# Performance work log

Hardware: AMD Instinct MI355X
Metric: run time of the kernel (lower is better)

The kernel has to match this reference:

```python
import jax, jax.numpy as jnp
import numpy as np

B, L, D = 32, 512, 128          # batch, seq_len, d_model (= num graph nodes N)
E, HS, DTR, U = 64, 64, 4, 32   # d_proj_E, d_proj_H (state), dt_rank, d_proj_U
R, K, DE, NH = 3, 3, 10, 4      # mamba layers, cheb order, d_e, heads
EPS = 1e-5


def _ln(x, g, b):
    m = jnp.mean(x, -1, keepdims=True)
    v = jnp.mean((x - m) ** 2, -1, keepdims=True)
    return (x - m) / jnp.sqrt(v + EPS) * g + b


def _mamba(x, in_w, conv_w, conv_b, xproj_w, dt_w, dt_b, Alog, Dp, out_w):
    b, l, _ = x.shape
    xz = x @ in_w                                  # (b,l,2E)
    xp, res = xz[..., :E], xz[..., E:]
    xc = jnp.transpose(xp, (0, 2, 1))              # (b,E,l)
    # causal depthwise conv: torch pads both sides by d_conv-1 then slices [:l]
    xc = jax.lax.conv_general_dilated(
        xc, conv_w, (1,), [(conv_w.shape[-1] - 1, 0)],
        dimension_numbers=('NCH', 'OIH', 'NCH'), feature_group_count=E)
    xc = xc + conv_b[None, :, None]
    xp = jax.nn.silu(jnp.transpose(xc, (0, 2, 1)))  # (b,l,E)
    xdbl = xp @ xproj_w                             # (b,l,DTR+2*HS)
    delta = jax.nn.softplus(xdbl[..., :DTR] @ dt_w + dt_b)        # (b,l,E)
    Bm = xdbl[..., DTR:DTR + HS]                                   # (b,l,HS)
    Cm = xdbl[..., DTR + HS:]                                      # (b,l,HS)
    A = -jnp.exp(Alog)                                             # (E,HS)
    dA = jnp.exp(delta[..., None] * A)                             # (b,l,E,HS)
    dBu = delta[..., None] * Bm[:, :, None, :] * xp[..., None]     # (b,l,E,HS)

    def step(s, t):
        dA_t, dBu_t, C_t = t
        s = dA_t * s + dBu_t
        return s, jnp.einsum('bdn,bn->bd', s, C_t)

    _, ys = jax.lax.scan(step, jnp.zeros((b, E, HS), x.dtype),
                         (jnp.swapaxes(dA, 0, 1), jnp.swapaxes(dBu, 0, 1),
                          jnp.swapaxes(Cm, 0, 1)))
    y = jnp.swapaxes(ys, 0, 1) + xp * Dp
    y = y * jax.nn.sigmoid(res)
    return y @ out_w


def _forward(x, mb_in_w, mb_conv_w, mb_conv_b, mb_xproj_w, mb_dt_w, mb_dt_b,
             mb_Alog, mb_D, mb_out_w, ln1_g, ln1_b, ln2_g, ln2_b,
             ffn_w1, ffn_b1, ffn_w2, ffn_b2,
             psi_emb, psi, W_q, W_k, attn_alpha, F_w, f_b, head_mix,
             head_w, head_b):
    # ---- bidirectional Mamba stack ----
    for i in range(R):
        f, bk = 2 * i, 2 * i + 1
        Y1 = _mamba(x, mb_in_w[f], mb_conv_w[f], mb_conv_b[f], mb_xproj_w[f],
                    mb_dt_w[f], mb_dt_b[f], mb_Alog[f], mb_D[f], mb_out_w[f])
        Y2 = jnp.flip(_mamba(jnp.flip(x, 1), mb_in_w[bk], mb_conv_w[bk],
                             mb_conv_b[bk], mb_xproj_w[bk], mb_dt_w[bk],
                             mb_dt_b[bk], mb_Alog[bk], mb_D[bk], mb_out_w[bk]), 1)
        Y3 = _ln(x + Y1 + Y2, ln1_g[i], ln1_b[i])
        Yp = jax.nn.relu(Y3 @ ffn_w1[i] + ffn_b1[i]) @ ffn_w2[i] + ffn_b2[i]
        x = _ln(Yp + Y3, ln2_g[i], ln2_b[i])
    h = jnp.transpose(x, (0, 2, 1))                # (B, N=D, L)
    # ---- MAGAC (deterministic single MC sample, eval, no edge drop) ----
    diff = psi_emb[:, None, :] - psi_emb[None, :, :]
    A_g = jax.nn.softmax(jnp.exp(-psi * jnp.sum(diff * diff, -1)), axis=1)
    Q = jnp.einsum('nd,dhm->nhm', psi_emb, W_q)
    Kt = jnp.einsum('nd,dhm->nhm', psi_emb, W_k)
    attn = jax.nn.softmax(jnp.einsum('nhd,mhd->hnm', Q, Kt)
                          / jnp.sqrt(jnp.asarray(DE, x.dtype)), axis=-1)
    alpha = jax.nn.sigmoid(attn_alpha)
    A_effs = alpha * A_g[None] + (1.0 - alpha) * attn   # (H,N,N)
    mix = jax.nn.softmax(head_mix)
    I = jnp.eye(D, dtype=x.dtype)
    out = jnp.zeros((x.shape[0], D), x.dtype)
    for hh in range(NH):
        A = A_effs[hh]
        sup = [I, A]
        for _ in range(2, K + 1):
            sup.append(2.0 * A @ sup[-1] - sup[-2])
        S = jnp.stack(sup, 0)                             # (K+1,N,N)
        Wf = jnp.einsum('nd,dkl->nkl', psi_emb, F_w[hh])  # (N,K+1,L)
        bf = psi_emb @ f_b[hh]                            # (N,)
        out_h = jnp.einsum('knm,bml,nkl->bn', S, h, Wf) + bf
        out = out + mix[hh] * out_h
    log_var = jnp.zeros_like(out)
    pred = out @ head_w + head_b                          # (B,1)
    return pred, log_var


def setup_inputs() -> dict:
    key = jax.random.key(0)
    ks = iter(jax.random.split(key, 40))
    nrm = lambda shp, s=0.05: (jax.random.normal(next(ks), shp, jnp.float32) * s)
    M = 2 * R
    base_Alog = jnp.log(jnp.arange(1, HS + 1, dtype=jnp.float32))
    inp = {
        'x': jax.random.normal(next(ks), (B, L, D), jnp.float32),
        'mb_in_w': nrm((M, D, 2 * E)),
        'mb_conv_w': nrm((M, E, 1, 3), 0.2),
        'mb_conv_b': jnp.zeros((M, E), jnp.float32),
        'mb_xproj_w': nrm((M, E, DTR + 2 * HS)),
        'mb_dt_w': nrm((M, DTR, E), 0.2),
        'mb_dt_b': jnp.zeros((M, E), jnp.float32),
        'mb_Alog': jnp.tile(base_Alog[None, None, :], (M, E, 1)),
        'mb_D': jnp.ones((M, E), jnp.float32),
        'mb_out_w': nrm((M, E, D)),
        'ln1_g': jnp.ones((R, D), jnp.float32),
        'ln1_b': jnp.zeros((R, D), jnp.float32),
        'ln2_g': jnp.ones((R, D), jnp.float32),
        'ln2_b': jnp.zeros((R, D), jnp.float32),
        'ffn_w1': nrm((R, D, U)),
        'ffn_b1': jnp.zeros((R, U), jnp.float32),
        'ffn_w2': nrm((R, U, D)),
        'ffn_b2': jnp.zeros((R, D), jnp.float32),
        'psi_emb': jax.random.normal(next(ks), (D, DE), jnp.float32),
        'psi': jnp.asarray(1.0, jnp.float32),
        'W_q': jax.random.normal(next(ks), (DE, NH, DE), jnp.float32),
        'W_k': jax.random.normal(next(ks), (DE, NH, DE), jnp.float32),
        'attn_alpha': jnp.asarray(0.5, jnp.float32),
        'F_w': nrm((NH, DE, K + 1, L), 0.05),
        'f_b': nrm((NH, DE), 1.0),
        'head_mix': jnp.ones((NH,), jnp.float32),
        'head_w': nrm((D, 1)),
        'head_b': jnp.zeros((1,), jnp.float32),
    }
    return inp


def reference(x, mb_in_w, mb_conv_w, mb_conv_b, mb_xproj_w, mb_dt_w, mb_dt_b,
              mb_Alog, mb_D, mb_out_w, ln1_g, ln1_b, ln2_g, ln2_b,
              ffn_w1, ffn_b1, ffn_w2, ffn_b2,
              psi_emb, psi, W_q, W_k, attn_alpha, F_w, f_b, head_mix,
              head_w, head_b):
    return _forward(x, mb_in_w, mb_conv_w, mb_conv_b, mb_xproj_w, mb_dt_w,
                    mb_dt_b, mb_Alog, mb_D, mb_out_w, ln1_g, ln1_b, ln2_g,
                    ln2_b, ffn_w1, ffn_b1, ffn_w2, ffn_b2, psi_emb, psi,
                    W_q, W_k, attn_alpha, F_w, f_b, head_mix, head_w, head_b)
```

## Files before the change

kernel.cpp:

```cpp
#include <hip/hip_runtime.h>
#include <hip/hip_bf16.h>


#define B_ 32
#define L_ 512
#define D_ 128
#define E_ 64
#define HS_ 64

#define OFF_X     0u
#define OFF_XZF   2097152u
#define OFF_XZB   4194304u
#define OFF_XPF   6291456u
#define OFF_XPB   7340032u
#define OFF_PKF   8388608u
#define OFF_PKB   10485760u
#define OFF_XBCF  12582912u
#define OFF_WFT   13631488u
#define OFF_XBCB  14680064u
#define OFF_STT   15728640u
#define OFF_AEFF  15990784u
#define OFF_YSF   16777216u
#define OFF_YSB   17825792u
#define OFF_V     2097152u
#define OFF_PART  12582912u
#define OFF_RED1  16777216u

__device__ __forceinline__ float sigf(float x) { return 1.f / (1.f + __expf(-x)); }
__device__ __forceinline__ unsigned int bf16r(float x) {
    unsigned int u = __float_as_uint(x);
    return (u + 0x7fffu + ((u >> 16) & 1u)) >> 16;
}

__device__ void role_wf(int bx0, int tid, const float* __restrict__ psi,
                        const float* __restrict__ F_w, float* __restrict__ WfT)
{
    const int idx = bx0 * 256 + tid;
    const int n = idx & 127, l = (idx >> 7) & 511, k = (idx >> 16) & 3, h = idx >> 18;
    float acc = 0.f;
#pragma unroll
    for (int d = 0; d < 10; ++d)
        acc = fmaf(psi[n * 10 + d], F_w[((h * 10 + d) * 4 + k) * 512 + l], acc);
    WfT[idx] = acc;
}

__device__ void role_qkaeff(int bx0, int tid, const float* __restrict__ psi,
                            const float* __restrict__ psis, const float* __restrict__ W_q,
                            const float* __restrict__ W_k, const float* __restrict__ attn_a,
                            float* __restrict__ Aeff, float* __restrict__ StT,
                            float* sQ2 , float* red2 )
{
    const int half = tid >> 7, mcol = tid & 127;
    const int unit = bx0 * 2 + half;
    const int h = unit >> 7, n = unit & 127;
    float Kreg[10];
#pragma unroll
    for (int d = 0; d < 10; ++d) Kreg[d] = 0.f;
#pragma unroll
    for (int d0 = 0; d0 < 10; ++d0) {
        const float pv = psi[mcol * 10 + d0];
#pragma unroll
        for (int d = 0; d < 10; ++d) Kreg[d] = fmaf(pv, W_k[(d0 * 4 + h) * 10 + d], Kreg[d]);
    }
    if (mcol < 10) {
        float qd = 0.f;
        for (int d0 = 0; d0 < 10; ++d0)
            qd = fmaf(psi[n * 10 + d0], W_q[(d0 * 4 + h) * 10 + mcol], qd);
        sQ2[half * 16 + mcol] = qd;
    }
    __syncthreads();
    float d2 = 0.f;
#pragma unroll
    for (int d = 0; d < 10; ++d) { const float df = psi[n * 10 + d] - psi[mcol * 10 + d]; d2 = fmaf(df, df, d2); }
    const float gv = __expf(-psis[0] * d2);
    float qv = 0.f;
#pragma unroll
    for (int d = 0; d < 10; ++d) qv = fmaf(sQ2[half * 16 + d], Kreg[d], qv);
    qv *= 0.3162277660168379332f;
    float* rd = red2 + half * 128;
    float r;
    rd[mcol] = gv; __syncthreads();
    for (int s = 64; s >= 1; s >>= 1) { if (mcol < s) rd[mcol] = fmaxf(rd[mcol], rd[mcol + s]); __syncthreads(); }
    r = rd[0]; __syncthreads();
    const float eg = __expf(gv - r);
    rd[mcol] = eg; __syncthreads();
    for (int s = 64; s >= 1; s >>= 1) { if (mcol < s) rd[mcol] += rd[mcol + s]; __syncthreads(); }
    const float gsum = rd[0]; __syncthreads();
    rd[mcol] = qv; __syncthreads();
    for (int s = 64; s >= 1; s >>= 1) { if (mcol < s) rd[mcol] = fmaxf(rd[mcol], rd[mcol + s]); __syncthreads(); }
    r = rd[0]; __syncthreads();
    const float eq = __expf(qv - r);
    rd[mcol] = eq; __syncthreads();
    for (int s = 64; s >= 1; s >>= 1) { if (mcol < s) rd[mcol] += rd[mcol + s]; __syncthreads(); }
    const float qsum = rd[0];
    const float al = sigf(attn_a[0]);
    const float aeff = al * (eg / gsum) + (1.f - al) * (eq / qsum);
    Aeff[h * 16384 + n * 128 + mcol] = aeff;
    StT[((h * 4 + 1) * 128 + mcol) * 128 + n] = aeff;
    StT[((h * 4 + 0) * 128 + mcol) * 128 + n] = (mcol == n) ? 1.f : 0.f;
}

__device__ void role_cheb(int bx0, int tid, const float* __restrict__ Aeff,
                          float* __restrict__ StT, int kk)
{
    const int h = bx0 >> 6;
    const int m0 = ((bx0 & 63) << 1) + (tid >> 7);
    const int n = tid & 127;
    const float* Ar = Aeff + h * 16384 + n * 128;
    const float* Sp = StT + ((h * 4 + kk - 1) * 128 + m0) * 128;
    float acc = 0.f;
#pragma unroll 8
    for (int p = 0; p < 128; ++p) acc = fmaf(Ar[p], Sp[p], acc);
    const float s2 = StT[((h * 4 + kk - 2) * 128 + m0) * 128 + n];
    StT[((h * 4 + kk) * 128 + m0) * 128 + n] = 2.f * acc - s2;
}

__global__ __launch_bounds__(256) void gemm_in2_kernel(
    const float* __restrict__ X, const float* __restrict__ WF, const float* __restrict__ WB,
    float* __restrict__ xzF, float* __restrict__ xzB)
{
    __shared__ float sxT[128][36];
    __shared__ float sw[2][16][128];
    const int tid = threadIdx.x;
    const int r0 = blockIdx.x * 32;
    for (int q = tid; q < 1024; q += 256) {
        const int r = q >> 5, k4 = q & 31;
        const float4 v = *(const float4*)&X[(size_t)(r0 + r) * 128 + k4 * 4];
        sxT[k4 * 4 + 0][r] = v.x; sxT[k4 * 4 + 1][r] = v.y;
        sxT[k4 * 4 + 2][r] = v.z; sxT[k4 * 4 + 3][r] = v.w;
    }
    const int wv = tid >> 6, lane = tid & 63;
    const int d = wv >> 1, ch = wv & 1;
    const int r4 = lane >> 4, c16 = lane & 15;
    float4 acc[8];
#pragma unroll
    for (int j = 0; j < 8; ++j) acc[j] = float4{0.f, 0.f, 0.f, 0.f};
    for (int ko = 0; ko < 128; ko += 16) {
        __syncthreads();
        for (int q = tid; q < 1024; q += 256) {
            const int dd = q >> 9, kk = (q >> 5) & 15, c4 = q & 31;
            *(float4*)&sw[dd][kk][c4 * 4] =
                *(const float4*)&((dd ? WB : WF)[(ko + kk) * 128 + c4 * 4]);
        }
        __syncthreads();
#pragma unroll
        for (int kk = 0; kk < 16; ++kk) {
            const float4 w4 = *(const float4*)&sw[d][kk][ch * 64 + c16 * 4];
            const float4 xa = *(const float4*)&sxT[ko + kk][r4 * 8];
            const float4 xb = *(const float4*)&sxT[ko + kk][r4 * 8 + 4];
            const float xs[8] = {xa.x, xa.y, xa.z, xa.w, xb.x, xb.y, xb.z, xb.w};
#pragma unroll
            for (int j = 0; j < 8; ++j) {
                acc[j].x = fmaf(xs[j], w4.x, acc[j].x);
                acc[j].y = fmaf(xs[j], w4.y, acc[j].y);
                acc[j].z = fmaf(xs[j], w4.z, acc[j].z);
                acc[j].w = fmaf(xs[j], w4.w, acc[j].w);
            }
        }
    }
    float* xz = d ? xzB : xzF;
#pragma unroll
    for (int j = 0; j < 8; ++j) {
        *(float4*)&xz[(r0 + r4 * 8 + j) * 128 + ch * 64 + c16 * 4] = acc[j];
    }
}

__global__ __launch_bounds__(256) void prep4_kernel(
    const float* __restrict__ xzF_, const float* __restrict__ xzB_,
    const float* __restrict__ conv_w, const float* __restrict__ conv_b,
    const float* __restrict__ xproj_w, const float* __restrict__ dt_w,
    const float* __restrict__ dt_b, int layer,
    float* __restrict__ xpF_, float* __restrict__ xpB_,
    unsigned int* __restrict__ xbcF_, unsigned int* __restrict__ xbcB_,
    float* __restrict__ pkF_, float* __restrict__ pkB_,
    const float* __restrict__ psi, const float* __restrict__ F_w, float* __restrict__ WfT,
    const float* __restrict__ Aeff, float* __restrict__ StT)
{
    __shared__ float sW[8448];
    __shared__ float sxp4[4][64][4];
    __shared__ float sdl4[4][4][4];
    const int tid = threadIdx.x, wv = tid >> 6, lane = tid & 63;
    if (blockIdx.x >= 2048) {
        const int bx0 = blockIdx.x - 2048;
        if (layer == 0) role_wf(bx0, tid, psi, F_w, WfT);
        else            role_cheb(bx0, tid, Aeff, StT, 3);
        return;
    }
    const int dir = (int)(blockIdx.x >= 1024);
    const int r0 = (blockIdx.x & 1023) * 16;
    const int b = r0 >> 9;
    const int m = layer * 2 + dir;
    const float* Wg = xproj_w + m * 8448;
    for (int q = tid; q < 2112; q += 256) ((float4*)sW)[q] = ((const float4*)Wg)[q];
    const float* xz = dir ? xzB_ : xzF_;
    float* xp  = dir ? xpB_  : xpF_;
    unsigned int* xbc = dir ? xbcB_ : xbcF_;
    float* pkx = dir ? pkB_  : pkF_;
    const float* cw = conv_w + m * 192 + lane * 3;
    const float cw0 = cw[0], cw1 = cw[1], cw2 = cw[2];
    const float cb  = conv_b[m * 64 + lane];
    const float dtb = dt_b[m * 64 + lane];
    const float* dwp = dt_w + m * 256;
    const float dw0 = dwp[lane], dw1 = dwp[64 + lane], dw2 = dwp[128 + lane], dw3 = dwp[192 + lane];
    float uu[4];
#pragma unroll
    for (int it = 0; it < 4; ++it) {
        const int row = r0 + wv * 4 + it;
        const int l = row & 511;
        const int l1 = dir ? l + 1 : l - 1;
        const int l2 = dir ? l + 2 : l - 2;
        float acc = cb;
        const float x0 = xz[(size_t)row * 128 + lane];
        const float x1 = (l1 >= 0 && l1 < 512) ? xz[(size_t)(b * 512 + l1) * 128 + lane] : 0.f;
        const float x2 = (l2 >= 0 && l2 < 512) ? xz[(size_t)(b * 512 + l2) * 128 + lane] : 0.f;
        acc += cw0 * x2 + cw1 * x1 + cw2 * x0;
        const float u = acc * sigf(acc);
        xp[row * 64 + lane] = u;
        uu[it] = u;
    }
    *(float4*)&sxp4[wv][lane][0] = float4{uu[0], uu[1], uu[2], uu[3]};
    __syncthreads();
    const int jdt = lane & 3;
    float aB[4] = {0.f, 0.f, 0.f, 0.f};
    float aC[4] = {0.f, 0.f, 0.f, 0.f};
    float adt[4] = {0.f, 0.f, 0.f, 0.f};
#pragma unroll 4
    for (int k = 0; k < 64; ++k) {
        const float wB = sW[k * 132 + 4 + lane];
        const float wC = sW[k * 132 + 68 + lane];
        const float wd = sW[k * 132 + jdt];
        const float4 xv = *(const float4*)&sxp4[wv][k][0];
        aB[0] = fmaf(xv.x, wB, aB[0]); aC[0] = fmaf(xv.x, wC, aC[0]); adt[0] = fmaf(xv.x, wd, adt[0]);
        aB[1] = fmaf(xv.y, wB, aB[1]); aC[1] = fmaf(xv.y, wC, aC[1]); adt[1] = fmaf(xv.y, wd, adt[1]);
        aB[2] = fmaf(xv.z, wB, aB[2]); aC[2] = fmaf(xv.z, wC, aC[2]); adt[2] = fmaf(xv.z, wd, adt[2]);
        aB[3] = fmaf(xv.w, wB, aB[3]); aC[3] = fmaf(xv.w, wC, aC[3]); adt[3] = fmaf(xv.w, wd, adt[3]);
    }
#pragma unroll
    for (int it = 0; it < 4; ++it) {
        const int row = r0 + wv * 4 + it;
        xbc[row * 64 + lane] = (bf16r(aC[it]) << 16) | bf16r(aB[it]);
        if (lane < 4) sdl4[wv][it][lane] = adt[it];
    }
#pragma unroll
    for (int it = 0; it < 4; ++it) {
        const int row = r0 + wv * 4 + it;
        float dpre = fmaf(sdl4[wv][it][0], dw0, dtb);
        dpre = fmaf(sdl4[wv][it][1], dw1, dpre);
        dpre = fmaf(sdl4[wv][it][2], dw2, dpre);
        dpre = fmaf(sdl4[wv][it][3], dw3, dpre);
        const float dlt = (dpre > 20.f) ? dpre : log1pf(__expf(dpre));
        ((float2*)pkx)[row * 64 + lane] = float2{dlt, dlt * uu[it]};
    }
}

__global__ __launch_bounds__(256, 4) void scan8_kernel(
    const unsigned int* __restrict__ xbcF, const unsigned int* __restrict__ xbcB,
    const float* __restrict__ pkF, const float* __restrict__ pkB,
    const float* __restrict__ AlogF, const float* __restrict__ AlogB,
    float* __restrict__ ysF, float* __restrict__ ysB,
    const float* __restrict__ psi, const float* __restrict__ psis,
    const float* __restrict__ W_q, const float* __restrict__ W_k,
    const float* __restrict__ attn_a, float* __restrict__ Aeff, float* __restrict__ StT)
{
    __shared__ unsigned int sbc[2][1024];
    __shared__ float spk[2][4][16][2];
    __shared__ float ytile[4][16][68];
    const int tid = threadIdx.x, wv = tid >> 6, lane = tid & 63;
    const int bx = blockIdx.x;
    if (bx >= 1024) {
        role_qkaeff(bx - 1024, tid, psi, psis, W_q, W_k, attn_a, Aeff, StT,
                    (float*)&sbc[1][0], (float*)&sbc[0][0]);
        return;
    }
    const int db = bx & 63;
    const int dir = db >> 5;
    const int b   = db & 31;
    const int e0  = (bx >> 6) * 4;
    const int e   = e0 + wv;
    const unsigned int* xbc = dir ? xbcB : xbcF;
    const float* pk  = dir ? pkB  : pkF;
    const float* Aw  = dir ? AlogB : AlogF;
    float* ys = dir ? ysB : ysF;
    const float a2 = -__expf(Aw[e * 64 + lane]) * 1.4426950408889634f;
    float s = 0.f;
    float* yrow = ys + (size_t)(b * 64 + e) * 512;

    const int psl = tid & 15, pw_ = tid >> 4;

#define STG_LOAD(RS)                                                              \
    {                                                                             \
        nb = *(const uint4*)(xbc + (size_t)(RS) * 64 + tid * 4);                  \
        if (tid < 64)                                                             \
            npp = *(const float2*)(pk + (size_t)((RS) + psl) * 128 + (e0 + pw_) * 2); \
    }
#define STG_WRITE(BUF)                                                            \
    {                                                                             \
        *(uint4*)(&sbc[BUF][tid * 4]) = nb;                                       \
        if (tid < 64) *(float2*)(&spk[BUF][pw_][psl][0]) = npp;                   \
    }

#define SCAN16(REV)                                                               \
    {                                                                             \
        const unsigned int* bc = &sbc[cur][0];                                    \
        const float* pq = &spk[cur][wv][0][0];                                    \
        _Pragma("unroll")                                                         \
        for (int j = 0; j < 8; ++j) {                                             \
            const int pj = (REV) ? 7 - j : j;                                     \
            const float4 pk4 = *(const float4*)(pq + pj * 4);                     \
            const int sA = (REV) ? 15 - 2 * j : 2 * j;                            \
            const int sB = (REV) ? 14 - 2 * j : 2 * j + 1;                        \
            const float dlA = (REV) ? pk4.z : pk4.x;                              \
            const float duA = (REV) ? pk4.w : pk4.y;                              \
            const float dlB = (REV) ? pk4.x : pk4.z;                              \
            const float duB = (REV) ? pk4.y : pk4.w;                              \
            const unsigned int bA = bc[sA * 64 + lane];                           \
            const float BnA = __uint_as_float(bA << 16);                          \
            const float CnA = __uint_as_float(bA & 0xffff0000u);                  \
            s = fmaf(__builtin_amdgcn_exp2f(dlA * a2), s, duA * BnA);             \
            ytile[wv][sA][lane] = s * CnA;                                        \
            const unsigned int bB = bc[sB * 64 + lane];                           \
            const float BnB = __uint_as_float(bB << 16);                          \
            const float CnB = __uint_as_float(bB & 0xffff0000u);                  \
            s = fmaf(__builtin_amdgcn_exp2f(dlB * a2), s, duB * BnB);             \
            ytile[wv][sB][lane] = s * CnB;                                        \
        }                                                                         \
    }

    {
        uint4 nb; float2 npp;
        const int rs0 = b * 512 + (dir ? 496 : 0);
        STG_LOAD(rs0);
        STG_WRITE(0);
    }
    __syncthreads();

    int cur = 0;
    const int rr = lane & 15, sg = lane >> 4;
    for (int t = 0; t < 32; ++t) {
        uint4 nb; float2 npp;
        const bool more = (t + 1) < 32;
        if (more) {
            const int rs = b * 512 + (dir ? (496 - (t + 1) * 16) : ((t + 1) * 16));
            STG_LOAD(rs);
        }
        if (dir == 0) { SCAN16(0) } else { SCAN16(1) }
        {
            const float* yt = &ytile[wv][rr][sg * 16];
            const float4 A0 = *(const float4*)yt;
            const float4 A1 = *(const float4*)(yt + 4);
            const float4 A2 = *(const float4*)(yt + 8);
            const float4 A3 = *(const float4*)(yt + 12);
            float p = ((A0.x + A0.y) + (A0.z + A0.w)) + ((A1.x + A1.y) + (A1.z + A1.w))
                    + ((A2.x + A2.y) + (A2.z + A2.w)) + ((A3.x + A3.y) + (A3.z + A3.w));
            p += __shfl_xor(p, 16);
            p += __shfl_xor(p, 32);
            if (lane < 16) {
                const int lg = dir ? (496 + rr - t * 16) : (t * 16 + rr);
                yrow[lg] = p;
            }
        }
        if (more) STG_WRITE(cur ^ 1);
        __syncthreads();
        cur ^= 1;
    }
#undef STG_LOAD
#undef STG_WRITE
#undef SCAN16
}

__global__ __launch_bounds__(256, 4) void opfn3_kernel(
    const float* __restrict__ ysF, const float* __restrict__ ysB,
    const float* __restrict__ xpF, const float* __restrict__ xpB,
    const float* __restrict__ xzF, const float* __restrict__ xzB,
    const float* __restrict__ Dp, int layer,
    const float* __restrict__ Xc, const float* __restrict__ out_w,
    const float* __restrict__ W1, const float* __restrict__ b1,
    const float* __restrict__ W2, const float* __restrict__ b2,
    const float* __restrict__ g1, const float* __restrict__ bb1,
    const float* __restrict__ g2, const float* __restrict__ bb2,
    float* __restrict__ xout,
    const float* __restrict__ WFn, const float* __restrict__ WBn,
    float* __restrict__ xzFo, float* __restrict__ xzBo,
    const float* __restrict__ Aeff, float* __restrict__ StT)
{
    __shared__ float smem[9216];
    float* syy = smem;
    float* sw  = smem + 4096;
    float* sh  = smem + 8192;
    const int tid = threadIdx.x;
    if (blockIdx.x >= 512) {
        role_cheb(blockIdx.x - 512, tid, Aeff, StT, 2);
        return;
    }
    const int r0 = blockIdx.x * 32;
    const int b = r0 >> 9, l0 = r0 & 511;
    const int wv = tid >> 6, lane = tid & 63;
    const float* WFp = out_w + (layer * 2) * 8192;
    const float* WBp = out_w + (layer * 2 + 1) * 8192;

    for (int q = tid; q < 1024; q += 256) {
        const int d = q >> 9, ee = (q >> 3) & 63, rq = q & 7;
        const float* ysp = d ? ysB : ysF;
        const float4 v = *(const float4*)&ysp[(size_t)(b * 64 + ee) * 512 + l0 + rq * 4];
        const float dv = Dp[(layer * 2 + d) * 64 + ee];
        const float* xpp = d ? xpB : xpF;
        const float* xzp = d ? xzB : xzF;
        const float vv[4] = {v.x, v.y, v.z, v.w};
#pragma unroll
        for (int j = 0; j < 4; ++j) {
            const int r = rq * 4 + j;
            const int row = r0 + r;
            const float u   = xpp[(size_t)row * 64 + ee];
            const float res = xzp[(size_t)row * 128 + 64 + ee];
            syy[r * 128 + d * 64 + ee] = (vv[j] + u * dv) * sigf(res);
        }
    }
    __syncthreads();

    float acc[8][2];
#pragma unroll
    for (int r = 0; r < 8; ++r) { acc[r][0] = 0.f; acc[r][1] = 0.f; }
#define OPSTEP8(COMP, J)                                                          \
        {                                                                         \
            const float w0 = sw[(kk + (J)) * 128 + lane];                         \
            const float w1 = sw[(kk + (J)) * 128 + lane + 64];                    \
            acc[0][0] = fmaf(y40.COMP, w0, acc[0][0]); acc[0][1] = fmaf(y40.COMP, w1, acc[0][1]); \
            acc[1][0] = fmaf(y41.COMP, w0, acc[1][0]); acc[1][1] = fmaf(y41.COMP, w1, acc[1][1]); \
            acc[2][0] = fmaf(y42.COMP, w0, acc[2][0]); acc[2][1] = fmaf(y42.COMP, w1, acc[2][1]); \
            acc[3][0] = fmaf(y43.COMP, w0, acc[3][0]); acc[3][1] = fmaf(y43.COMP, w1, acc[3][1]); \
            acc[4][0] = fmaf(y44.COMP, w0, acc[4][0]); acc[4][1] = fmaf(y44.COMP, w1, acc[4][1]); \
            acc[5][0] = fmaf(y45.COMP, w0, acc[5][0]); acc[5][1] = fmaf(y45.COMP, w1, acc[5][1]); \
            acc[6][0] = fmaf(y46.COMP, w0, acc[6][0]); acc[6][1] = fmaf(y46.COMP, w1, acc[6][1]); \
            acc[7][0] = fmaf(y47.COMP, w0, acc[7][0]); acc[7][1] = fmaf(y47.COMP, w1, acc[7][1]); \
        }
#define GEMM_CHUNK8(SRC, KO)                                                      \
    _Pragma("unroll")                                                             \
    for (int kk = 0; kk < 32; kk += 4) {                                          \
        const float4 y40 = *(const float4*)&(SRC)[(wv * 8 + 0) * 128 + (KO) + kk];\
        const float4 y41 = *(const float4*)&(SRC)[(wv * 8 + 1) * 128 + (KO) + kk];\
        const float4 y42 = *(const float4*)&(SRC)[(wv * 8 + 2) * 128 + (KO) + kk];\
        const float4 y43 = *(const float4*)&(SRC)[(wv * 8 + 3) * 128 + (KO) + kk];\
        const float4 y44 = *(const float4*)&(SRC)[(wv * 8 + 4) * 128 + (KO) + kk];\
        const float4 y45 = *(const float4*)&(SRC)[(wv * 8 + 5) * 128 + (KO) + kk];\
        const float4 y46 = *(const float4*)&(SRC)[(wv * 8 + 6) * 128 + (KO) + kk];\
        const float4 y47 = *(const float4*)&(SRC)[(wv * 8 + 7) * 128 + (KO) + kk];\
        OPSTEP8(x, 0) OPSTEP8(y, 1) OPSTEP8(z, 2) OPSTEP8(w, 3)                  \
    }
    for (int koi = 0; koi < 4; ++koi) {
        if (koi) __syncthreads();
        for (int q = tid; q < 1024; q += 256) {
            const int kk = q >> 5, c4 = q & 31;
            const int kg = koi * 32 + kk;
            *(float4*)&sw[kk * 128 + c4 * 4] = (kg < 64)
                ? *(const float4*)&WFp[kg * 128 + c4 * 4]
                : *(const float4*)&WBp[(kg - 64) * 128 + c4 * 4];
        }
        __syncthreads();
        GEMM_CHUNK8(syy, koi * 32);
    }
    __syncthreads();
    for (int q = tid; q < 1024; q += 256) ((float4*)sw)[q] = ((const float4*)W1)[q];
#pragma unroll
    for (int r = 0; r < 8; ++r) {
        const int rl = wv * 8 + r;
        const int row = r0 + rl;
        float v0 = acc[r][0] + Xc[(size_t)row * 128 + lane];
        float v1 = acc[r][1] + Xc[(size_t)row * 128 + lane + 64];
        float sum = v0 + v1, sq = v0 * v0 + v1 * v1;
#pragma unroll
        for (int o = 32; o >= 1; o >>= 1) { sum += __shfl_xor(sum, o); sq += __shfl_xor(sq, o); }
        const float mean = sum * (1.f / 128.f);
        const float var = sq * (1.f / 128.f) - mean * mean;
        const float rs = rsqrtf(var + 1e-5f);
        syy[rl * 128 + lane]      = (v0 - mean) * rs * g1[lane] + bb1[lane];
        syy[rl * 128 + lane + 64] = (v1 - mean) * rs * g1[lane + 64] + bb1[lane + 64];
    }
    __syncthreads();
    {
        const int r = tid >> 3, ug = (tid & 7) * 4;
        float h0 = b1[ug], h1 = b1[ug + 1], h2 = b1[ug + 2], h3 = b1[ug + 3];
#pragma unroll 8
        for (int k = 0; k < 128; ++k) {
            const float xv = syy[r * 128 + k];
            h0 = fmaf(xv, sw[k * 32 + ug], h0);
            h1 = fmaf(xv, sw[k * 32 + ug + 1], h1);
            h2 = fmaf(xv, sw[k * 32 + ug + 2], h2);
            h3 = fmaf(xv, sw[k * 32 + ug + 3], h3);
        }
        sh[r * 32 + ug]     = fmaxf(h0, 0.f);
        sh[r * 32 + ug + 1] = fmaxf(h1, 0.f);
        sh[r * 32 + ug + 2] = fmaxf(h2, 0.f);
        sh[r * 32 + ug + 3] = fmaxf(h3, 0.f);
    }
    __syncthreads();
    for (int q = tid; q < 1024; q += 256) ((float4*)sw)[q] = ((const float4*)W2)[q];
    __syncthreads();
    float xr[8][2];
#pragma unroll
    for (int r = 0; r < 8; ++r) {
        const int rl = wv * 8 + r;
        float a0 = b2[lane], a1 = b2[lane + 64];
#pragma unroll 8
        for (int k = 0; k < 32; ++k) {
            const float hv = sh[rl * 32 + k];
            a0 = fmaf(hv, sw[k * 128 + lane], a0);
            a1 = fmaf(hv, sw[k * 128 + lane + 64], a1);
        }
        const float v0 = a0 + syy[rl * 128 + lane];
        const float v1 = a1 + syy[rl * 128 + lane + 64];
        float sum = v0 + v1, sq = v0 * v0 + v1 * v1;
#pragma unroll
        for (int o = 32; o >= 1; o >>= 1) { sum += __shfl_xor(sum, o); sq += __shfl_xor(sq, o); }
        const float mean = sum * (1.f / 128.f);
        const float var = sq * (1.f / 128.f) - mean * mean;
        const float rs = rsqrtf(var + 1e-5f);
        const int row = r0 + rl;
        const float o0 = (v0 - mean) * rs * g2[lane] + bb2[lane];
        const float o1 = (v1 - mean) * rs * g2[lane + 64] + bb2[lane + 64];
        xout[(size_t)row * 128 + lane]      = o0;
        xout[(size_t)row * 128 + lane + 64] = o1;
        xr[r][0] = o0; xr[r][1] = o1;
    }
    if (WFn == nullptr) return;
    __syncthreads();
    float* sxr = syy;
#pragma unroll
    for (int r = 0; r < 8; ++r) {
        sxr[(wv * 8 + r) * 128 + lane]      = xr[r][0];
        sxr[(wv * 8 + r) * 128 + lane + 64] = xr[r][1];
    }
    for (int c = 0; c < 8; ++c) {
        const int dd = c >> 2, ko = (c & 3) * 32;
        const float* Wn = dd ? WBn : WFn;
        for (int q = tid; q < 1024; q += 256) {
            const int kk = q >> 5, c4 = q & 31;
            *(float4*)&sw[kk * 128 + c4 * 4] = *(const float4*)&Wn[(ko + kk) * 128 + c4 * 4];
        }
        __syncthreads();
        if ((c & 3) == 0) {
#pragma unroll
            for (int r = 0; r < 8; ++r) { acc[r][0] = 0.f; acc[r][1] = 0.f; }
        }
        GEMM_CHUNK8(sxr, ko);
        if ((c & 3) == 3) {
            float* xzo = dd ? xzBo : xzFo;
#pragma unroll
            for (int r = 0; r < 8; ++r) {
                const int row = r0 + wv * 8 + r;
                xzo[(size_t)row * 128 + lane]      = acc[r][0];
                xzo[(size_t)row * 128 + lane + 64] = acc[r][1];
            }
        }
        __syncthreads();
    }
#undef OPSTEP8
#undef GEMM_CHUNK8
}

__global__ __launch_bounds__(256) void head_v4_kernel(
    const float* __restrict__ StT, const float* __restrict__ WfT, const float* __restrict__ hmix,
    float* __restrict__ V)
{
    const float m0 = hmix[0], m1 = hmix[1], m2 = hmix[2], m3 = hmix[3];
    const float mxx = fmaxf(fmaxf(m0, m1), fmaxf(m2, m3));
    const float e0 = __expf(m0 - mxx), e1 = __expf(m1 - mxx), e2 = __expf(m2 - mxx), e3 = __expf(m3 - mxx);
    const float inv = 1.f / (e0 + e1 + e2 + e3);
    const float mixv[4] = {e0 * inv, e1 * inv, e2 * inv, e3 * inv};
    const int tid = threadIdx.x;
    const int lt = blockIdx.x & 63, mm = blockIdx.x >> 6;
    const int n4 = tid & 31, mh = tid >> 5;
    const int m = mm * 8 + mh;
    const int l0 = lt * 8, n0 = n4 * 4;
    float4 sv[16];
#pragma unroll
    for (int h = 0; h < 4; ++h) {
        const float mx = mixv[h];
#pragma unroll
        for (int k = 0; k < 4; ++k) {
            const float4 v = *(const float4*)&StT[(size_t)((h * 4 + k) * 128 + m) * 128 + n0];
            sv[h * 4 + k] = float4{v.x * mx, v.y * mx, v.z * mx, v.w * mx};
        }
    }
#pragma unroll
    for (int j = 0; j < 8; ++j) {
        const int l = l0 + j;
        float4 acc = {0.f, 0.f, 0.f, 0.f};
#pragma unroll
        for (int hk = 0; hk < 16; ++hk) {
            const float4 w = *(const float4*)&WfT[(size_t)(hk * 512 + l) * 128 + n0];
            acc.x = fmaf(sv[hk].x, w.x, acc.x);
            acc.y = fmaf(sv[hk].y, w.y, acc.y);
            acc.z = fmaf(sv[hk].z, w.z, acc.z);
            acc.w = fmaf(sv[hk].w, w.w, acc.w);
        }
        *(float4*)&V[(size_t)(l * 128 + m) * 128 + n0] = acc;
    }
}

__global__ __launch_bounds__(256) void head_ctr_kernel(
    const float* __restrict__ Xf, const float* __restrict__ V, float* __restrict__ partial)
{
    __shared__ float sx[32][128];
    const int l = blockIdx.x, tid = threadIdx.x;
    const int n = tid & 127, mh = tid >> 7;
    for (int q = tid; q < 1024; q += 256) {
        const int b = q >> 5, m4 = q & 31;
        *(float4*)&sx[b][m4 * 4] = *(const float4*)&Xf[(size_t)(b * 512 + l) * 128 + m4 * 4];
    }
    __syncthreads();
    float acc[32];
#pragma unroll
    for (int b = 0; b < 32; ++b) acc[b] = 0.f;
    const float* vp = V + (size_t)(l * 128 + mh * 64) * 128 + n;
    for (int mm = 0; mm < 64; ++mm) {
        const float v = vp[(size_t)mm * 128];
        const int m = mh * 64 + mm;
#pragma unroll
        for (int b = 0; b < 32; ++b) acc[b] = fmaf(sx[b][m], v, acc[b]);
    }
#pragma unroll
    for (int b = 0; b < 32; ++b)
        partial[(size_t)((l * 2 + mh) * 32 + b) * 128 + n] = acc[b];
}

__global__ __launch_bounds__(128) void head_red_kernel(
    const float* __restrict__ partial, float* __restrict__ red1)
{
    const int b = blockIdx.x >> 5, cs = blockIdx.x & 31, n = threadIdx.x;
    const float* p = partial + ((size_t)(cs * 32) * 32 + b) * 128 + n;
    float s = 0.f;
#pragma unroll 8
    for (int c = 0; c < 32; ++c) s += p[(size_t)c * 4096];
    red1[(b * 32 + cs) * 128 + n] = s;
}

__global__ __launch_bounds__(128) void head_out_kernel(
    const float* __restrict__ red1, const float* __restrict__ psi,
    const float* __restrict__ f_b, const float* __restrict__ hmix,
    const float* __restrict__ head_w, const float* __restrict__ head_b, float* __restrict__ out)
{
    __shared__ float red[128];
    const int b = blockIdx.x, n = threadIdx.x;
    const float m0 = hmix[0], m1 = hmix[1], m2 = hmix[2], m3 = hmix[3];
    const float mxx = fmaxf(fmaxf(m0, m1), fmaxf(m2, m3));
    const float e0 = __expf(m0 - mxx), e1 = __expf(m1 - mxx), e2 = __expf(m2 - mxx), e3 = __expf(m3 - mxx);
    const float inv = 1.f / (e0 + e1 + e2 + e3);
    const float mixv[4] = {e0 * inv, e1 * inv, e2 * inv, e3 * inv};
    float s = 0.f;
#pragma unroll
    for (int h = 0; h < 4; ++h) {
        float t = 0.f;
#pragma unroll
        for (int d = 0; d < 10; ++d) t = fmaf(psi[n * 10 + d], f_b[h * 10 + d], t);
        s = fmaf(mixv[h], t, s);
    }
#pragma unroll 8
    for (int cs = 0; cs < 32; ++cs) s += red1[(b * 32 + cs) * 128 + n];
    red[n] = s * head_w[n];
    __syncthreads();
    for (int st = 64; st >= 1; st >>= 1) { if (n < st) red[n] += red[n + st]; __syncthreads(); }
    if (n == 0) out[b] = red[0] + head_b[0];
    out[32 + b * 128 + n] = 0.f;
}

extern "C" void kernel_launch(void* const* d_in, const int* in_sizes, int n_in,
                              void* d_out, int out_size, void* d_ws, size_t ws_size,
                              hipStream_t stream) {
    const float* x_in    = (const float*)d_in[0];
    const float* in_w    = (const float*)d_in[1];
    const float* conv_w  = (const float*)d_in[2];
    const float* conv_b  = (const float*)d_in[3];
    const float* xproj_w = (const float*)d_in[4];
    const float* dt_w    = (const float*)d_in[5];
    const float* dt_b    = (const float*)d_in[6];
    const float* Alog    = (const float*)d_in[7];
    const float* Dp      = (const float*)d_in[8];
    const float* out_w   = (const float*)d_in[9];
    const float* ln1_g   = (const float*)d_in[10];
    const float* ln1_b   = (const float*)d_in[11];
    const float* ln2_g   = (const float*)d_in[12];
    const float* ln2_b   = (const float*)d_in[13];
    const float* ffn_w1  = (const float*)d_in[14];
    const float* ffn_b1  = (const float*)d_in[15];
    const float* ffn_w2  = (const float*)d_in[16];
    const float* ffn_b2  = (const float*)d_in[17];
    const float* psi_emb = (const float*)d_in[18];
    const float* psi_s   = (const float*)d_in[19];
    const float* W_q     = (const float*)d_in[20];
    const float* W_k     = (const float*)d_in[21];
    const float* attn_a  = (const float*)d_in[22];
    const float* F_w     = (const float*)d_in[23];
    const float* f_b     = (const float*)d_in[24];
    const float* hmix    = (const float*)d_in[25];
    const float* head_w  = (const float*)d_in[26];
    const float* head_b  = (const float*)d_in[27];
    float* ws = (float*)d_ws;
    float* outp = (float*)d_out;

    gemm_in2_kernel<<<512, 256, 0, stream>>>(
        x_in, in_w, in_w + 16384, ws + OFF_XZF, ws + OFF_XZB);
    for (int i = 0; i < 3; ++i) {
        const float* xcur = (i == 0) ? x_in : (ws + OFF_X);
        const int mF = 2 * i, mB = 2 * i + 1;
        const int prep_grid = (i == 0) ? 6144 : (i == 1) ? 2304 : 2048;
        prep4_kernel<<<prep_grid, 256, 0, stream>>>(
            ws + OFF_XZF, ws + OFF_XZB, conv_w, conv_b, xproj_w, dt_w, dt_b, i,
            ws + OFF_XPF, ws + OFF_XPB,
            (unsigned int*)(ws + OFF_XBCF), (unsigned int*)(ws + OFF_XBCB),
            ws + OFF_PKF, ws + OFF_PKB,
            psi_emb, F_w, ws + OFF_WFT, ws + OFF_AEFF, ws + OFF_STT);
        const int scan_grid = (i == 0) ? 1280 : 1024;
        scan8_kernel<<<scan_grid, 256, 0, stream>>>(
            (const unsigned int*)(ws + OFF_XBCF), (const unsigned int*)(ws + OFF_XBCB),
            ws + OFF_PKF, ws + OFF_PKB,
            Alog + mF * 4096, Alog + mB * 4096, ws + OFF_YSF, ws + OFF_YSB,
            psi_emb, psi_s, W_q, W_k, attn_a, ws + OFF_AEFF, ws + OFF_STT);
        const float* WFn = (i < 2) ? (in_w + (2 * i + 2) * 16384) : nullptr;
        const float* WBn = (i < 2) ? (in_w + (2 * i + 3) * 16384) : nullptr;
        const int opfn_grid = (i == 0) ? 768 : 512;
        opfn3_kernel<<<opfn_grid, 256, 0, stream>>>(
            ws + OFF_YSF, ws + OFF_YSB, ws + OFF_XPF, ws + OFF_XPB, ws + OFF_XZF, ws + OFF_XZB,
            Dp, i, xcur, out_w,
            ffn_w1 + i * 4096, ffn_b1 + i * 32, ffn_w2 + i * 4096, ffn_b2 + i * 128,
            ln1_g + i * 128, ln1_b + i * 128, ln2_g + i * 128, ln2_b + i * 128,
            ws + OFF_X, WFn, WBn, ws + OFF_XZF, ws + OFF_XZB,
            ws + OFF_AEFF, ws + OFF_STT);
    }
    head_v4_kernel<<<1024, 256, 0, stream>>>(ws + OFF_STT, ws + OFF_WFT, hmix, ws + OFF_V);
    head_ctr_kernel<<<512, 256, 0, stream>>>(ws + OFF_X, ws + OFF_V, ws + OFF_PART);
    head_red_kernel<<<1024, 128, 0, stream>>>(ws + OFF_PART, ws + OFF_RED1);
    head_out_kernel<<<32, 128, 0, stream>>>(
        ws + OFF_RED1, psi_emb, f_b, hmix, head_w, head_b, outp);
}
```

Measured before the change: 479.3 us.

## Fold head V computation into last opfn launch and store V as bf16

The separate head_v4 kernel is removed. Its work now runs as extra blocks (1024 of them) appended to the final layer's opfn3 launch, so it overlaps with the output/FFN work and saves a kernel launch. V is also written as packed bf16 instead of fp32, which halves the traffic of the large V tensor between the producer and head_ctr. This lowers the precision of V and relocates its buffer to a new workspace offset, which has to avoid aliasing live buffers.

Result: faster. 448.6 us (median of 2 runs) (-6.4%).

```diff
diff --git a/kernel.cpp b/kernel.cpp
--- a/kernel.cpp
+++ b/kernel.cpp
@@ -22,7 +22,7 @@
 #define OFF_AEFF  15990784u
 #define OFF_YSF   16777216u
 #define OFF_YSB   17825792u
-#define OFF_V     2097152u
+#define OFF_VB    8388608u
 #define OFF_PART  12582912u
 #define OFF_RED1  16777216u
 
@@ -113,6 +113,47 @@
     for (int p = 0; p < 128; ++p) acc = fmaf(Ar[p], Sp[p], acc);
     const float s2 = StT[((h * 4 + kk - 2) * 128 + m0) * 128 + n];
     StT[((h * 4 + kk) * 128 + m0) * 128 + n] = 2.f * acc - s2;
+}
+
+__device__ void role_v4(int bx0, int tid, const float* __restrict__ StT,
+                        const float* __restrict__ WfT, const float* __restrict__ hmix,
+                        unsigned int* __restrict__ Vb)
+{
+    const float m0 = hmix[0], m1 = hmix[1], m2 = hmix[2], m3 = hmix[3];
+    const float mxx = fmaxf(fmaxf(m0, m1), fmaxf(m2, m3));
+    const float e0 = __expf(m0 - mxx), e1 = __expf(m1 - mxx), e2 = __expf(m2 - mxx), e3 = __expf(m3 - mxx);
+    const float inv = 1.f / (e0 + e1 + e2 + e3);
+    const float mixv[4] = {e0 * inv, e1 * inv, e2 * inv, e3 * inv};
+    const int lt = bx0 & 63, mm = bx0 >> 6;
+    const int n4 = tid & 31, mh = tid >> 5;
+    const int m = mm * 8 + mh;
+    const int l0 = lt * 8, n0 = n4 * 4;
+    float4 sv[16];
+#pragma unroll
+    for (int h = 0; h < 4; ++h) {
+        const float mx = mixv[h];
+#pragma unroll
+        for (int k = 0; k < 4; ++k) {
+            const float4 v = *(const float4*)&StT[(size_t)((h * 4 + k) * 128 + m) * 128 + n0];
+            sv[h * 4 + k] = float4{v.x * mx, v.y * mx, v.z * mx, v.w * mx};
+        }
+    }
+#pragma unroll
+    for (int j = 0; j < 8; ++j) {
+        const int l = l0 + j;
+        float4 acc = {0.f, 0.f, 0.f, 0.f};
+#pragma unroll
+        for (int hk = 0; hk < 16; ++hk) {
+            const float4 w = *(const float4*)&WfT[(size_t)(hk * 512 + l) * 128 + n0];
+            acc.x = fmaf(sv[hk].x, w.x, acc.x);
+            acc.y = fmaf(sv[hk].y, w.y, acc.y);
+            acc.z = fmaf(sv[hk].z, w.z, acc.z);
+            acc.w = fmaf(sv[hk].w, w.w, acc.w);
+        }
+        const uint2 p = uint2{(bf16r(acc.y) << 16) | bf16r(acc.x),
+                              (bf16r(acc.w) << 16) | bf16r(acc.z)};
+        *(uint2*)&Vb[(size_t)(l * 128 + m) * 64 + (n0 >> 1)] = p;
+    }
 }
 
 __global__ __launch_bounds__(256) void gemm_in2_kernel(
@@ -381,7 +422,9 @@
     float* __restrict__ xout,
     const float* __restrict__ WFn, const float* __restrict__ WBn,
     float* __restrict__ xzFo, float* __restrict__ xzBo,
-    const float* __restrict__ Aeff, float* __restrict__ StT)
+    const float* __restrict__ Aeff, float* __restrict__ StT,
+    const float* __restrict__ WfT, const float* __restrict__ hmix,
+    unsigned int* __restrict__ Vb)
 {
     __shared__ float smem[9216];
     float* syy = smem;
@@ -389,7 +432,9 @@
     float* sh  = smem + 8192;
     const int tid = threadIdx.x;
     if (blockIdx.x >= 512) {
-        role_cheb(blockIdx.x - 512, tid, Aeff, StT, 2);
+        const int bx0 = blockIdx.x - 512;
+        if (layer == 0) role_cheb(bx0, tid, Aeff, StT, 2);
+        else            role_v4(bx0, tid, StT, WfT, hmix, Vb);
         return;
     }
     const int r0 = blockIdx.x * 32;
@@ -557,48 +602,9 @@
 #undef GEMM_CHUNK8
 }
 
-__global__ __launch_bounds__(256) void head_v4_kernel(
-    const float* __restrict__ StT, const float* __restrict__ WfT, const float* __restrict__ hmix,
-    float* __restrict__ V)
-{
-    const float m0 = hmix[0], m1 = hmix[1], m2 = hmix[2], m3 = hmix[3];
-    const float mxx = fmaxf(fmaxf(m0, m1), fmaxf(m2, m3));
-    const float e0 = __expf(m0 - mxx), e1 = __expf(m1 - mxx), e2 = __expf(m2 - mxx), e3 = __expf(m3 - mxx);
-    const float inv = 1.f / (e0 + e1 + e2 + e3);
-    const float mixv[4] = {e0 * inv, e1 * inv, e2 * inv, e3 * inv};
-    const int tid = threadIdx.x;
-    const int lt = blockIdx.x & 63, mm = blockIdx.x >> 6;
-    const int n4 = tid & 31, mh = tid >> 5;
-    const int m = mm * 8 + mh;
-    const int l0 = lt * 8, n0 = n4 * 4;
-    float4 sv[16];
-#pragma unroll
-    for (int h = 0; h < 4; ++h) {
-        const float mx = mixv[h];
-#pragma unroll
-        for (int k = 0; k < 4; ++k) {
-            const float4 v = *(const float4*)&StT[(size_t)((h * 4 + k) * 128 + m) * 128 + n0];
-            sv[h * 4 + k] = float4{v.x * mx, v.y * mx, v.z * mx, v.w * mx};
-        }
-    }
-#pragma unroll
-    for (int j = 0; j < 8; ++j) {
-        const int l = l0 + j;
-        float4 acc = {0.f, 0.f, 0.f, 0.f};
-#pragma unroll
-        for (int hk = 0; hk < 16; ++hk) {
-            const float4 w = *(const float4*)&WfT[(size_t)(hk * 512 + l) * 128 + n0];
-            acc.x = fmaf(sv[hk].x, w.x, acc.x);
-            acc.y = fmaf(sv[hk].y, w.y, acc.y);
-            acc.z = fmaf(sv[hk].z, w.z, acc.z);
-            acc.w = fmaf(sv[hk].w, w.w, acc.w);
-        }
-        *(float4*)&V[(size_t)(l * 128 + m) * 128 + n0] = acc;
-    }
-}
-
 __global__ __launch_bounds__(256) void head_ctr_kernel(
-    const float* __restrict__ Xf, const float* __restrict__ V, float* __restrict__ partial)
+    const float* __restrict__ Xf, const unsigned int* __restrict__ Vb,
+    float* __restrict__ partial)
 {
     __shared__ float sx[32][128];
     const int l = blockIdx.x, tid = threadIdx.x;
@@ -611,9 +617,11 @@
     float acc[32];
 #pragma unroll
     for (int b = 0; b < 32; ++b) acc[b] = 0.f;
-    const float* vp = V + (size_t)(l * 128 + mh * 64) * 128 + n;
+    const unsigned int* vp = Vb + (size_t)(l * 128 + mh * 64) * 64 + (n >> 1);
+    const bool hi = (n & 1);
     for (int mm = 0; mm < 64; ++mm) {
-        const float v = vp[(size_t)mm * 128];
+        const unsigned int u = vp[(size_t)mm * 64];
+        const float v = __uint_as_float(hi ? (u & 0xffff0000u) : (u << 16));
         const int m = mh * 64 + mm;
 #pragma unroll
         for (int b = 0; b < 32; ++b) acc[b] = fmaf(sx[b][m], v, acc[b]);
@@ -717,17 +725,18 @@
             psi_emb, psi_s, W_q, W_k, attn_a, ws + OFF_AEFF, ws + OFF_STT);
         const float* WFn = (i < 2) ? (in_w + (2 * i + 2) * 16384) : nullptr;
         const float* WBn = (i < 2) ? (in_w + (2 * i + 3) * 16384) : nullptr;
-        const int opfn_grid = (i == 0) ? 768 : 512;
+        const int opfn_grid = (i == 0) ? 768 : (i == 1) ? 512 : 1536;
         opfn3_kernel<<<opfn_grid, 256, 0, stream>>>(
             ws + OFF_YSF, ws + OFF_YSB, ws + OFF_XPF, ws + OFF_XPB, ws + OFF_XZF, ws + OFF_XZB,
             Dp, i, xcur, out_w,
             ffn_w1 + i * 4096, ffn_b1 + i * 32, ffn_w2 + i * 4096, ffn_b2 + i * 128,
             ln1_g + i * 128, ln1_b + i * 128, ln2_g + i * 128, ln2_b + i * 128,
             ws + OFF_X, WFn, WBn, ws + OFF_XZF, ws + OFF_XZB,
-            ws + OFF_AEFF, ws + OFF_STT);
-    }
-    head_v4_kernel<<<1024, 256, 0, stream>>>(ws + OFF_STT, ws + OFF_WFT, hmix, ws + OFF_V);
-    head_ctr_kernel<<<512, 256, 0, stream>>>(ws + OFF_X, ws + OFF_V, ws + OFF_PART);
+            ws + OFF_AEFF, ws + OFF_STT,
+            ws + OFF_WFT, hmix, (unsigned int*)(ws + OFF_VB));
+    }
+    head_ctr_kernel<<<512, 256, 0, stream>>>(
+        ws + OFF_X, (const unsigned int*)(ws + OFF_VB), ws + OFF_PART);
     head_red_kernel<<<1024, 128, 0, stream>>>(ws + OFF_PART, ws + OFF_RED1);
     head_out_kernel<<<32, 128, 0, stream>>>(
         ws + OFF_RED1, psi_emb, f_b, hmix, head_w, head_b, outp);
```
